# Kernel tuning notes

Hardware: AMD Instinct MI355X
Metric: run time of the kernel (lower is better)

Reference implementation:

```python
import jax, jax.numpy as jnp
import numpy as np

B, C, H, W = 32, 512, 40, 40
NC = 20
STRIDE = 32
CONF_THRESH = 0.3
NMS_THRESH = 0.5


def setup_inputs() -> dict:
    key = jax.random.key(0)
    ks = jax.random.split(key, 7)
    # 0.02 scale on weights keeps sigmoid/exp in a realistic, non-saturated range
    return {
        "feat": jax.random.normal(ks[0], (B, C, H, W), dtype=jnp.float32),
        "w_obj": jax.random.normal(ks[1], (1, C), dtype=jnp.float32) * 0.02,
        "b_obj": jnp.zeros((1,), dtype=jnp.float32),
        "w_cls": jax.random.normal(ks[2], (NC, C), dtype=jnp.float32) * 0.02,
        "b_cls": jnp.zeros((NC,), dtype=jnp.float32),
        "w_reg": jax.random.normal(ks[3], (4, C), dtype=jnp.float32) * 0.02,
        "b_reg": jnp.zeros((4,), dtype=jnp.float32),
    }


def _pairwise_iou(b):  # b: [N,4] xyxy
    area = (b[:, 2] - b[:, 0]) * (b[:, 3] - b[:, 1])
    x1 = jnp.maximum(b[:, None, 0], b[None, :, 0])
    y1 = jnp.maximum(b[:, None, 1], b[None, :, 1])
    x2 = jnp.minimum(b[:, None, 2], b[None, :, 2])
    y2 = jnp.minimum(b[:, None, 3], b[None, :, 3])
    inter = jnp.maximum(x2 - x1, 0.0) * jnp.maximum(y2 - y1, 0.0)
    union = area[:, None] + area[None, :] - inter
    return inter / union


def _nms_single(boxes, scores, labels, conf_mask):
    # Greedy per-class NMS with fixed shapes (keep mask), matching the
    # original: suppression happens only among boxes of the same class
    # that pass conf_thresh, in descending score order.
    N = boxes.shape[0]
    order = jnp.argsort(-scores)
    b = boxes[order]
    l = labels[order]
    v = conf_mask[order]
    iou = _pairwise_iou(b)  # [N,N]
    idx = jnp.arange(N)
    later = idx[None, :] > idx[:, None]
    sup = (iou > NMS_THRESH) & (l[:, None] == l[None, :]) & later

    def body(i, keep):
        # if box i is still kept, suppress all later same-class overlaps
        return keep & ~(sup[i] & keep[i])

    keep_sorted = jax.lax.fori_loop(0, N, body, v)
    return jnp.zeros((N,), dtype=bool).at[order].set(keep_sorted)


def reference(feat, w_obj, b_obj, w_cls, b_cls, w_reg, b_reg):
    Bn, Cc, Hh, Ww = feat.shape
    N = Hh * Ww
    # permute(0,2,3,1).flatten(1,2) -> [B, H*W, C]
    x = feat.transpose(0, 2, 3, 1).reshape(Bn, N, Cc)
    # 1x1 convs == per-cell linear layers
    obj = jnp.einsum("bnc,oc->bno", x, w_obj) + b_obj  # [B,N,1]
    cls = jnp.einsum("bnc,oc->bno", x, w_cls) + b_cls  # [B,N,NC]
    reg = jnp.einsum("bnc,oc->bno", x, w_reg) + b_reg  # [B,N,4]
    # decode_boxes
    gy, gx = jnp.meshgrid(jnp.arange(Hh), jnp.arange(Ww), indexing="ij")
    grid = jnp.stack([gx, gy], axis=-1).reshape(-1, 2).astype(feat.dtype)  # [N,2]
    ctr = (jax.nn.sigmoid(reg[..., :2]) + grid) * STRIDE
    wh = jnp.exp(reg[..., 2:]) * STRIDE
    boxes = jnp.concatenate([ctr - wh * 0.5, ctr + wh * 0.5], axis=-1)  # [B,N,4]
    # scores = sqrt(sigmoid(obj) * sigmoid(cls)); per-cell best class
    sc = jnp.sqrt(jax.nn.sigmoid(obj) * jax.nn.sigmoid(cls))  # [B,N,NC]
    scores = sc.max(axis=-1)
    labels = jnp.argmax(sc, axis=-1)
    conf_mask = scores > CONF_THRESH
    keep = jax.vmap(_nms_single)(boxes, scores, labels, conf_mask)  # [B,N]
    out = jnp.concatenate(
        [jnp.where(keep[..., None], boxes, 0.0),
         jnp.where(keep, scores, 0.0)[..., None]],
        axis=-1,
    )  # [B,N,5]
    return out, labels, keep
```

## Files before the change

kernel.cpp:

```cpp
#include <hip/hip_runtime.h>
#include <stdint.h>
#include <stddef.h>

#define Bn 32
#define Cc 512
#define Hh 40
#define Ww 40
#define Npix 1600
#define NCx 20
#define NCELL (Bn*Npix)
#define CONF 0.3f
#define NMS_T 0.5f
#define NOUT 25

#define CB 64
#define BPI 25
#define NWAVE 4
#define CR (Cc/NWAVE)
#define FB 8

#define WS_WT     0
#define WS_BOXES  (WS_WT + (size_t)NOUT*Cc)
#define WS_SCORES (WS_BOXES + (size_t)NCELL*4)
#define WS_LABELS (WS_SCORES + (size_t)NCELL)

__device__ __forceinline__ float sigmoidf_(float x) {
    return 1.0f / (1.0f + expf(-x));
}

__global__ __launch_bounds__(64) void k0_pack(
    const float* __restrict__ w_obj, const float* __restrict__ w_cls,
    const float* __restrict__ w_reg, float* __restrict__ Wt)
{
    int c = blockIdx.x * 64 + threadIdx.x;
    if (c < Cc) {
        Wt[c] = w_obj[c];
        #pragma unroll
        for (int o = 0; o < NCx; ++o) Wt[(size_t)(1 + o) * Cc + c] = w_cls[o * Cc + c];
        #pragma unroll
        for (int o = 0; o < 4; ++o)   Wt[(size_t)(21 + o) * Cc + c] = w_reg[o * Cc + c];
    }
}

__device__ __forceinline__ void ld_batch(float dst[FB], const float* __restrict__ fp,
                                         int base) {
    #pragma unroll
    for (int t = 0; t < FB; ++t) dst[t] = fp[(size_t)(base + t) * Npix];
}

__device__ __forceinline__ void fma_batch(float acc[NOUT], const float x[FB],
                                          const float* __restrict__ wt0, int base) {
    #pragma unroll
    for (int o = 0; o < NOUT; ++o) {
        const float* wr = wt0 + (size_t)o * Cc + base;
        #pragma unroll
        for (int t = 0; t < FB; ++t)
            acc[o] = fmaf(x[t], wr[t], acc[o]);
    }
}

__global__ __launch_bounds__(256) void k1_fused(
    const float* __restrict__ feat, const float* __restrict__ Wt,
    const float* __restrict__ b_obj, const float* __restrict__ b_cls,
    const float* __restrict__ b_reg,
    float* __restrict__ out, float* __restrict__ ws_boxes,
    float* __restrict__ ws_scores, int* __restrict__ ws_labels)
{
    __shared__ float red[NWAVE][NOUT][CB];

    const int tid = threadIdx.x;
    const int w   = __builtin_amdgcn_readfirstlane(tid >> 6);
    const int l   = tid & 63;
    const int b   = blockIdx.x / BPI;
    const int j   = blockIdx.x % BPI;
    const int n0  = j * CB;

    {
        const float* fp  = feat + (size_t)b * (Cc * Npix) + (size_t)(w * CR) * Npix + (n0 + l);
        const float* wt0 = Wt + w * CR;

        float acc[NOUT];
        #pragma unroll
        for (int o = 0; o < NOUT; ++o) acc[o] = 0.f;

        float xa[FB], xb[FB];
        ld_batch(xa, fp, 0);
        int base = 0;
        for (; base < CR - 2 * FB; base += 2 * FB) {
            ld_batch(xb, fp, base + FB);
            fma_batch(acc, xa, wt0, base);
            ld_batch(xa, fp, base + 2 * FB);
            fma_batch(acc, xb, wt0, base + FB);
        }
        ld_batch(xb, fp, base + FB);
        fma_batch(acc, xa, wt0, base);
        fma_batch(acc, xb, wt0, base + FB);

        #pragma unroll
        for (int o = 0; o < NOUT; ++o) red[w][o][l] = acc[o];
    }
    __syncthreads();

    if (tid < CB) {
        float v[NOUT];
        #pragma unroll
        for (int o = 0; o < NOUT; ++o) v[o] = red[0][o][tid];
        #pragma unroll
        for (int ch = 1; ch < NWAVE; ++ch) {
            #pragma unroll
            for (int o = 0; o < NOUT; ++o) v[o] += red[ch][o][tid];
        }

        float obj = v[0] + b_obj[0];
        float m = -1e30f; int label = 0;
        #pragma unroll
        for (int o = 0; o < NCx; ++o) {
            float cv = v[1 + o] + b_cls[o];
            if (cv > m) { m = cv; label = o; }
        }
        float r0 = v[21] + b_reg[0], r1 = v[22] + b_reg[1];
        float r2 = v[23] + b_reg[2], r3 = v[24] + b_reg[3];

        int n = n0 + tid;
        int g = b * Npix + n;
        int gy = n / Ww, gx = n % Ww;
        float cx = (sigmoidf_(r0) + (float)gx) * 32.0f;
        float cy = (sigmoidf_(r1) + (float)gy) * 32.0f;
        float bw = expf(r2) * 32.0f;
        float bh = expf(r3) * 32.0f;
        float x1 = cx - bw * 0.5f, y1 = cy - bh * 0.5f;
        float x2 = cx + bw * 0.5f, y2 = cy + bh * 0.5f;
        float score = sqrtf(sigmoidf_(obj) * sigmoidf_(m));

        ((float4*)ws_boxes)[g] = make_float4(x1, y1, x2, y2);
        ws_scores[g] = score;
        ws_labels[g] = label;

        float* orow = out + (size_t)g * 5;
        orow[0] = 0.f; orow[1] = 0.f; orow[2] = 0.f; orow[3] = 0.f; orow[4] = 0.f;
        out[(size_t)NCELL * 5 + g] = (float)label;
        out[(size_t)NCELL * 6 + g] = 0.f;
    }
}

#define KSUP 320
#define WUMAX ((KSUP + 31) / 32)

__global__ __launch_bounds__(256) void k3_nms(
    const float4* __restrict__ ws_boxes, const float* __restrict__ ws_scores,
    const int* __restrict__ ws_labels, float* __restrict__ out)
{
    __shared__ unsigned int cnt;
    __shared__ unsigned long long keys[2048];
    __shared__ float bx1[Npix], by1[Npix], bx2[Npix], by2[Npix], bar[Npix];
    __shared__ unsigned int sup[KSUP * WUMAX];
    __shared__ unsigned int keepbits[WUMAX];

    const int tid = threadIdx.x;
    const int b   = blockIdx.x / NCx;
    const int cls = blockIdx.x % NCx;
    const int gbase = b * Npix;

    if (tid == 0) cnt = 0;
    __syncthreads();

    for (int n = tid; n < Npix; n += 256) {
        float s = ws_scores[gbase + n];
        if (s > CONF && ws_labels[gbase + n] == cls) {
            unsigned int pos = atomicAdd(&cnt, 1u);
            unsigned int sb = __float_as_uint(s);
            keys[pos] = ((unsigned long long)(~sb) << 32) | (unsigned int)n;
        }
    }
    __syncthreads();
    const int k = (int)cnt;
    if (k == 0) return;

    int M = 2; while (M < k) M <<= 1;
    for (int s = tid; s < M; s += 256) if (s >= k) keys[s] = ~0ull;
    __syncthreads();

    for (int sz = 2; sz <= M; sz <<= 1) {
        for (int st = sz >> 1; st > 0; st >>= 1) {
            for (int t = tid; t < M; t += 256) {
                int p = t ^ st;
                if (p > t) {
                    unsigned long long a = keys[t], c = keys[p];
                    bool up = ((t & sz) == 0);
                    if (up ? (a > c) : (a < c)) { keys[t] = c; keys[p] = a; }
                }
            }
            __syncthreads();
        }
    }

    for (int s = tid; s < k; s += 256) {
        int n = (int)(unsigned int)keys[s];
        float4 bx = ws_boxes[gbase + n];
        bx1[s] = bx.x; by1[s] = bx.y; bx2[s] = bx.z; by2[s] = bx.w;
        bar[s] = (bx.z - bx.x) * (bx.w - bx.y);
    }
    __syncthreads();

    if (k <= KSUP) {
        const int wu = (k + 31) >> 5;
        for (int t = tid; t < k * wu; t += 256) {
            int i = t / wu, w = t - (t / wu) * wu;
            unsigned int bits = 0;
            int j0 = w << 5;
            float xi1 = bx1[i], yi1 = by1[i], xi2 = bx2[i], yi2 = by2[i], ai = bar[i];
            for (int jj = 0; jj < 32; ++jj) {
                int j = j0 + jj;
                if (j > i && j < k) {
                    float xx1 = fmaxf(xi1, bx1[j]);
                    float yy1 = fmaxf(yi1, by1[j]);
                    float xx2 = fminf(xi2, bx2[j]);
                    float yy2 = fminf(yi2, by2[j]);
                    float inter = fmaxf(xx2 - xx1, 0.f) * fmaxf(yy2 - yy1, 0.f);
                    float uni = ai + bar[j] - inter;
                    if (inter / uni > NMS_T) bits |= (1u << jj);
                }
            }
            sup[i * wu + w] = bits;
        }
        if (tid < wu) {
            int rem = k - (tid << 5);
            keepbits[tid] = (rem >= 32) ? 0xFFFFFFFFu : ((1u << rem) - 1u);
        }
        __syncthreads();

        if (tid < 64) {
            for (int i = 0; i < k; ++i) {
                unsigned int cur = keepbits[i >> 5];
                if ((cur >> (i & 31)) & 1u) {
                    if (tid < wu) keepbits[tid] &= ~sup[i * wu + tid];
                }
            }
            unsigned int* keepF = sup;
            for (int s2 = tid; s2 < k; s2 += 64)
                keepF[s2] = (keepbits[s2 >> 5] >> (s2 & 31)) & 1u;
        }
        __syncthreads();
    } else {
        unsigned int* keepF = sup;
        for (int s = tid; s < k; s += 256) keepF[s] = 1u;
        __syncthreads();
        for (int i = 0; i < k; ++i) {
            __syncthreads();
            if (keepF[i]) {
                float xi1 = bx1[i], yi1 = by1[i], xi2 = bx2[i], yi2 = by2[i], ai = bar[i];
                for (int j = i + 1 + tid; j < k; j += 256) {
                    float xx1 = fmaxf(xi1, bx1[j]);
                    float yy1 = fmaxf(yi1, by1[j]);
                    float xx2 = fminf(xi2, bx2[j]);
                    float yy2 = fminf(yi2, by2[j]);
                    float inter = fmaxf(xx2 - xx1, 0.f) * fmaxf(yy2 - yy1, 0.f);
                    float uni = ai + bar[j] - inter;
                    if (inter / uni > NMS_T) keepF[j] = 0u;
                }
            }
        }
        __syncthreads();
    }

    unsigned int* keepF = sup;
    for (int s = tid; s < k; s += 256) {
        if (keepF[s]) {
            int n = (int)(unsigned int)keys[s];
            unsigned int sb = ~(unsigned int)(keys[s] >> 32);
            float sc = __uint_as_float(sb);
            float* orow = out + (size_t)(gbase + n) * 5;
            orow[0] = bx1[s]; orow[1] = by1[s];
            orow[2] = bx2[s]; orow[3] = by2[s];
            orow[4] = sc;
            out[(size_t)NCELL * 6 + gbase + n] = 1.0f;
        }
    }
}

extern "C" void kernel_launch(void* const* d_in, const int* in_sizes, int n_in,
                              void* d_out, int out_size, void* d_ws, size_t ws_size,
                              hipStream_t stream) {
    const float* feat  = (const float*)d_in[0];
    const float* w_obj = (const float*)d_in[1];
    const float* b_obj = (const float*)d_in[2];
    const float* w_cls = (const float*)d_in[3];
    const float* b_cls = (const float*)d_in[4];
    const float* w_reg = (const float*)d_in[5];
    const float* b_reg = (const float*)d_in[6];
    float* out = (float*)d_out;
    float* ws  = (float*)d_ws;

    float* Wt     = ws + WS_WT;
    float* boxes  = ws + WS_BOXES;
    float* scores = ws + WS_SCORES;
    int*   labels = (int*)(ws + WS_LABELS);

    k0_pack<<<(Cc + 63) / 64, 64, 0, stream>>>(w_obj, w_cls, w_reg, Wt);
    k1_fused<<<Bn * BPI, 256, 0, stream>>>(feat, Wt, b_obj, b_cls, b_reg,
                                           out, boxes, scores, labels);
    k3_nms<<<Bn * NCx, 256, 0, stream>>>((const float4*)boxes, scores, labels, out);
}
```

Measured before the change: 248.4 us.

## Split 1x1 conv outputs across waves instead of splitting channels

Each wave now computes 7 of the 28 (padded) output rows over all 512 channels, where before each wave covered a quarter of the channels for all 25 outputs. This removes the cross-wave shared-memory reduction and cuts accumulator registers per thread from 25 to 7, which may raise occupancy. The cost is that every wave now reads the full feature column for its 64 pixels, so each block issues four times the feature loads, relying on L1/L2 hits. The weight matrix is padded with zero rows to 28.

```diff
diff --git a/kernel.cpp b/kernel.cpp
--- a/kernel.cpp
+++ b/kernel.cpp
@@ -12,15 +12,17 @@
 #define CONF 0.3f
 #define NMS_T 0.5f
 #define NOUT 25
+#define NROW 28
 
 #define CB 64
 #define BPI 25
 #define NWAVE 4
-#define CR (Cc/NWAVE)
+#define OPW 7
+#define CHUNK 128
 #define FB 8
 
 #define WS_WT     0
-#define WS_BOXES  (WS_WT + (size_t)NOUT*Cc)
+#define WS_BOXES  (WS_WT + (size_t)NROW*Cc)
 #define WS_SCORES (WS_BOXES + (size_t)NCELL*4)
 #define WS_LABELS (WS_SCORES + (size_t)NCELL)
 
@@ -39,23 +41,24 @@
         for (int o = 0; o < NCx; ++o) Wt[(size_t)(1 + o) * Cc + c] = w_cls[o * Cc + c];
         #pragma unroll
         for (int o = 0; o < 4; ++o)   Wt[(size_t)(21 + o) * Cc + c] = w_reg[o * Cc + c];
-    }
-}
-
-__device__ __forceinline__ void ld_batch(float dst[FB], const float* __restrict__ fp,
-                                         int base) {
+        #pragma unroll
+        for (int o = 25; o < NROW; ++o) Wt[(size_t)o * Cc + c] = 0.f;
+    }
+}
+
+__device__ __forceinline__ void ld8(float dst[FB], const float* __restrict__ fp, int base) {
     #pragma unroll
     for (int t = 0; t < FB; ++t) dst[t] = fp[(size_t)(base + t) * Npix];
 }
 
-__device__ __forceinline__ void fma_batch(float acc[NOUT], const float x[FB],
-                                          const float* __restrict__ wt0, int base) {
+__device__ __forceinline__ void fma7(float acc[OPW], const float x[FB],
+                                     const float* __restrict__ wbase, int base) {
     #pragma unroll
-    for (int o = 0; o < NOUT; ++o) {
-        const float* wr = wt0 + (size_t)o * Cc + base;
-        #pragma unroll
-        for (int t = 0; t < FB; ++t)
-            acc[o] = fmaf(x[t], wr[t], acc[o]);
+    for (int t = 0; t < FB; ++t) {
+        float xv = x[t];
+        #pragma unroll
+        for (int o = 0; o < OPW; ++o)
+            acc[o] = fmaf(xv, wbase[(size_t)o * Cc + base + t], acc[o]);
     }
 }
 
@@ -66,7 +69,7 @@
     float* __restrict__ out, float* __restrict__ ws_boxes,
     float* __restrict__ ws_scores, int* __restrict__ ws_labels)
 {
-    __shared__ float red[NWAVE][NOUT][CB];
+    __shared__ float red[NROW][CB];
 
     const int tid = threadIdx.x;
     const int w   = __builtin_amdgcn_readfirstlane(tid >> 6);
@@ -76,40 +79,45 @@
     const int n0  = j * CB;
 
     {
-        const float* fp  = feat + (size_t)b * (Cc * Npix) + (size_t)(w * CR) * Npix + (n0 + l);
-        const float* wt0 = Wt + w * CR;
-
-        float acc[NOUT];
-        #pragma unroll
-        for (int o = 0; o < NOUT; ++o) acc[o] = 0.f;
-
-        float xa[FB], xb[FB];
-        ld_batch(xa, fp, 0);
-        int base = 0;
-        for (; base < CR - 2 * FB; base += 2 * FB) {
-            ld_batch(xb, fp, base + FB);
-            fma_batch(acc, xa, wt0, base);
-            ld_batch(xa, fp, base + 2 * FB);
-            fma_batch(acc, xb, wt0, base + FB);
-        }
-        ld_batch(xb, fp, base + FB);
-        fma_batch(acc, xa, wt0, base);
-        fma_batch(acc, xb, wt0, base + FB);
-
-        #pragma unroll
-        for (int o = 0; o < NOUT; ++o) red[w][o][l] = acc[o];
+        const float* fp    = feat + (size_t)b * (Cc * Npix) + (n0 + l);
+        const float* wbase = Wt + (size_t)(w * OPW) * Cc;
+
+        float tot[OPW];
+        #pragma unroll
+        for (int ch = 0; ch < Cc / CHUNK; ++ch) {
+            const int c0 = ch * CHUNK;
+            float acc[OPW];
+            #pragma unroll
+            for (int o = 0; o < OPW; ++o) acc[o] = 0.f;
+
+            float xa[FB], xb[FB];
+            ld8(xa, fp, c0);
+            int base = c0;
+            #pragma unroll
+            for (int g = 0; g < CHUNK / (2 * FB) - 1; ++g) {
+                ld8(xb, fp, base + FB);
+                fma7(acc, xa, wbase, base);
+                ld8(xa, fp, base + 2 * FB);
+                fma7(acc, xb, wbase, base + FB);
+                base += 2 * FB;
+            }
+            ld8(xb, fp, base + FB);
+            fma7(acc, xa, wbase, base);
+            fma7(acc, xb, wbase, base + FB);
+
+            #pragma unroll
+            for (int o = 0; o < OPW; ++o)
+                tot[o] = (ch == 0) ? acc[o] : (tot[o] + acc[o]);
+        }
+        #pragma unroll
+        for (int o = 0; o < OPW; ++o) red[w * OPW + o][l] = tot[o];
     }
     __syncthreads();
 
     if (tid < CB) {
         float v[NOUT];
         #pragma unroll
-        for (int o = 0; o < NOUT; ++o) v[o] = red[0][o][tid];
-        #pragma unroll
-        for (int ch = 1; ch < NWAVE; ++ch) {
-            #pragma unroll
-            for (int o = 0; o < NOUT; ++o) v[o] += red[ch][o][tid];
-        }
+        for (int o = 0; o < NOUT; ++o) v[o] = red[o][tid];
 
         float obj = v[0] + b_obj[0];
         float m = -1e30f; int label = 0;
```

New measurement: 244.6 us. About the same (-1.5%).
